# Kernel optimization log

Measured on AMD Instinct MI355X. Metric: run time of the kernel, lower is better.

The kernel has to match this reference:

```python
import jax, jax.numpy as jnp
import numpy as np

N1, E1 = 102400, 300000
N2, E2 = 10240, 40960
N3, E3 = 1024, 4096
G = 64
D = 256   # node_dim == hidden_dim (forced by where(M==0, x, M))
B = 64    # bond_dim
DEPTHS = (3, 3, 4)


def _make_edges(rng, n_nodes, n_edges):
    # build mirrored directed edges so every edge has an exact reverse
    half = n_edges // 2
    u = rng.integers(0, n_nodes, half)
    v = rng.integers(0, n_nodes, half)
    src = np.concatenate([u, v])
    dst = np.concatenate([v, u])
    rev = np.concatenate([np.arange(half, n_edges), np.arange(0, half)])
    return np.stack([src, dst]).astype(np.int64), rev.astype(np.int64)


def _linear_params(key, fan_in, fan_out):
    k1, k2 = jax.random.split(key)
    s = 1.0 / np.sqrt(fan_in)
    W = jax.random.uniform(k1, (fan_in, fan_out), jnp.float32, -s, s)
    b = jax.random.uniform(k2, (fan_out,), jnp.float32, -s, s)
    return W, b


def setup_inputs() -> dict:
    rng = np.random.default_rng(0)
    key = jax.random.key(0)
    ks = jax.random.split(key, 16)

    ei1, rev1 = _make_edges(rng, N1, E1)
    ei2, rev2 = _make_edges(rng, N2, E2)
    ei3, rev3 = _make_edges(rng, N3, E3)

    inp = {
        "x": jax.random.normal(ks[0], (N1, D), jnp.float32),
        "edge_attr1": jax.random.normal(ks[1], (E1, B), jnp.float32),
        "edge_attr2": jax.random.normal(ks[2], (E2, B), jnp.float32),
        "edge_attr3": jax.random.normal(ks[3], (E3, B), jnp.float32),
        "edge_index1": jnp.asarray(ei1), "rev_edge_index1": jnp.asarray(rev1),
        "edge_index2": jnp.asarray(ei2), "rev_edge_index2": jnp.asarray(rev2),
        "edge_index3": jnp.asarray(ei3), "rev_edge_index3": jnp.asarray(rev3),
        "batch1_2": jnp.asarray(np.repeat(np.arange(N2), N1 // N2)),
        "batch2": jnp.asarray(np.repeat(np.arange(N3), N2 // N3)),
        "batch3": jnp.asarray(np.repeat(np.arange(G), N3 // G)),
    }
    kidx = 4
    for lvl in (1, 2, 3):
        Wi, bi = _linear_params(ks[kidx], D + B, D); kidx += 1
        Wh, bh = _linear_params(ks[kidx], D, D); kidx += 1
        Wo, bo = _linear_params(ks[kidx], D + D, D); kidx += 1
        inp[f"Wi{lvl}"], inp[f"bi{lvl}"] = Wi, bi
        inp[f"Wh{lvl}"], inp[f"bh{lvl}"] = Wh, bh
        inp[f"Wo{lvl}"], inp[f"bo{lvl}"] = Wo, bo
    return inp


def _bmp(x, src, dst, rev, ea, Wi, bi, Wh, bh, Wo, bo, depth):
    # BondMessagePassing.forward (dropout is identity in eval)
    n = x.shape[0]
    H0 = jax.nn.relu(jnp.concatenate([x[src], ea], axis=1) @ Wi + bi)  # [E, D]
    H = H0
    for _ in range(depth - 1):
        agg = jax.ops.segment_sum(H, dst, num_segments=n)              # [N, D]
        M = agg[src] - H[rev]
        H = jax.nn.relu(H0 + M @ Wh + bh)
    M = jax.ops.segment_sum(H, dst, num_segments=n)
    M = jnp.where(jnp.sum(M, axis=1, keepdims=True) == 0, x, M)
    return jax.nn.relu(jnp.concatenate([x, M], axis=1) @ Wo + bo)


def _mean_pool(h, seg, n):
    s = jax.ops.segment_sum(h, seg, num_segments=n)
    c = jax.ops.segment_sum(jnp.ones((h.shape[0], 1), h.dtype), seg, num_segments=n)
    return s / jnp.maximum(c, 1.0)


def reference(x, edge_attr1, edge_attr2, edge_attr3,
              edge_index1, rev_edge_index1, edge_index2, rev_edge_index2,
              edge_index3, rev_edge_index3, batch1_2, batch2, batch3,
              Wi1, bi1, Wh1, bh1, Wo1, bo1,
              Wi2, bi2, Wh2, bh2, Wo2, bo2,
              Wi3, bi3, Wh3, bh3, Wo3, bo3):
    h1 = _bmp(x, edge_index1[0], edge_index1[1], rev_edge_index1, edge_attr1,
              Wi1, bi1, Wh1, bh1, Wo1, bo1, DEPTHS[0])
    x2 = _mean_pool(h1, batch1_2, N2)
    h2 = _bmp(x2, edge_index2[0], edge_index2[1], rev_edge_index2, edge_attr2,
              Wi2, bi2, Wh2, bh2, Wo2, bo2, DEPTHS[1])
    x3 = _mean_pool(h2, batch2, N3)
    h3 = _bmp(x3, edge_index3[0], edge_index3[1], rev_edge_index3, edge_attr3,
              Wi3, bi3, Wh3, bh3, Wo3, bo3, DEPTHS[2])
    out = _mean_pool(h3, batch3, G)  # [G, D] subgraph3_pooled
    return out
```

## Files before the change

### kernel.cpp

```cpp
#include <hip/hip_runtime.h>
#include <stdint.h>

typedef __bf16 bf16;
typedef __bf16 bf16x4 __attribute__((ext_vector_type(4)));
typedef __bf16 bf16x8 __attribute__((ext_vector_type(8)));
typedef float  f32x4  __attribute__((ext_vector_type(4)));

__device__ __forceinline__ int clampi(int v, int n) { return (v < 0 || v >= n) ? 0 : v; }

__device__ __forceinline__ void gload16(const void* g, void* l) {
  __builtin_amdgcn_global_load_lds((const __attribute__((address_space(1))) void*)g,
                                   (__attribute__((address_space(3))) void*)l, 16, 0, 0);
}

__global__ void wtcvt_kernel(const float* __restrict__ W, bf16* __restrict__ Wt, int K) {
  int idx = blockIdx.x * 256 + threadIdx.x;
  if (idx >= K * 256) return;
  int k = idx >> 8, n = idx & 255;
  Wt[(size_t)n * K + k] = (bf16)W[idx];
}

__global__ void hist_kernel(const int* __restrict__ dst, int E, int* __restrict__ cnt, int N) {
  int e = blockIdx.x * 256 + threadIdx.x;
  if (e < E) atomicAdd(&cnt[clampi(dst[e], N)], 1);
}

__global__ void scan_block_kernel(const int* __restrict__ cnt, int N,
                                  int* __restrict__ incl, int* __restrict__ bsums) {
  __shared__ int sd[256];
  int t = threadIdx.x, bid = blockIdx.x;
  int base = bid * 1024 + t * 4;
  int v0 = (base + 0 < N) ? cnt[base + 0] : 0;
  int v1 = (base + 1 < N) ? cnt[base + 1] : 0;
  int v2 = (base + 2 < N) ? cnt[base + 2] : 0;
  int v3 = (base + 3 < N) ? cnt[base + 3] : 0;
  int s1 = v0 + v1, s2 = s1 + v2, s3 = s2 + v3;
  sd[t] = s3;
  __syncthreads();
  for (int off = 1; off < 256; off <<= 1) {
    int x = 0;
    if (t >= off) x = sd[t - off];
    __syncthreads();
    sd[t] += x;
    __syncthreads();
  }
  int excl = sd[t] - s3;
  if (base + 0 < N) incl[base + 0] = excl + v0;
  if (base + 1 < N) incl[base + 1] = excl + s1;
  if (base + 2 < N) incl[base + 2] = excl + s2;
  if (base + 3 < N) incl[base + 3] = excl + s3;
  if (t == 255) bsums[bid] = sd[255];
}

__global__ void scan_sums_kernel(const int* __restrict__ bsums, int nb, int* __restrict__ bexcl) {
  __shared__ int sd[256];
  int t = threadIdx.x;
  int v = (t < nb) ? bsums[t] : 0;
  sd[t] = v;
  __syncthreads();
  for (int off = 1; off < 256; off <<= 1) {
    int x = 0;
    if (t >= off) x = sd[t - off];
    __syncthreads();
    sd[t] += x;
    __syncthreads();
  }
  if (t < nb) bexcl[t] = sd[t] - v;
}

__global__ void scan_add_kernel(const int* __restrict__ incl, const int* __restrict__ bexcl,
                                int N, int* __restrict__ offs) {
  int i = blockIdx.x * 256 + threadIdx.x;
  if (i < N) offs[i + 1] = incl[i] + bexcl[i >> 10];
  if (i == 0) offs[0] = 0;
}

__global__ void scatter_kernel(const int* __restrict__ dst, int E, const int* __restrict__ offs,
                               int* __restrict__ cursor, int* __restrict__ elist, int N) {
  int e = blockIdx.x * 256 + threadIdx.x;
  if (e < E) {
    int d = clampi(dst[e], N);
    int p = atomicAdd(&cursor[d], 1);
    elist[offs[d] + p] = e;
  }
}

template <int WHERE, int XF32>
__global__ void segsum_kernel(const bf16* __restrict__ H, const int* __restrict__ elist,
                              const int* __restrict__ offs, const float* __restrict__ xf,
                              const bf16* __restrict__ xb, bf16* __restrict__ out, int N) {
  int lane = threadIdx.x & 63;
  int node = blockIdx.x * 4 + (threadIdx.x >> 6);
  if (node >= N) return;
  int beg = offs[node], end = offs[node + 1];
  float a0 = 0.f, a1 = 0.f, a2 = 0.f, a3 = 0.f;
  for (int p = beg; p < end; ++p) {
    int e = elist[p];
    bf16x4 v = ((const bf16x4*)(H + (size_t)e * 256))[lane];
    a0 += (float)v[0]; a1 += (float)v[1]; a2 += (float)v[2]; a3 += (float)v[3];
  }
  if (WHERE) {
    float s = a0 + a1 + a2 + a3;
    for (int off = 1; off < 64; off <<= 1) s += __shfl_xor(s, off);
    if (s == 0.f) {
      bf16x4 o;
      if (XF32) {
        float4 xv = ((const float4*)(xf))[(size_t)node * 64 + lane];
        o[0] = (bf16)xv.x; o[1] = (bf16)xv.y; o[2] = (bf16)xv.z; o[3] = (bf16)xv.w;
      } else {
        o = ((const bf16x4*)(xb + (size_t)node * 256))[lane];
      }
      ((bf16x4*)(out + (size_t)node * 256))[lane] = o;
      return;
    }
  }
  bf16x4 o = {(bf16)a0, (bf16)a1, (bf16)a2, (bf16)a3};
  ((bf16x4*)(out + (size_t)node * 256))[lane] = o;
}

template <int OUTF32>
__global__ void pool_kernel(const bf16* __restrict__ h, bf16* __restrict__ outb,
                            float* __restrict__ outf, int Nout, int cnt) {
  int lane = threadIdx.x & 63;
  int node = blockIdx.x * 4 + (threadIdx.x >> 6);
  if (node >= Nout) return;
  float a0 = 0.f, a1 = 0.f, a2 = 0.f, a3 = 0.f;
  size_t base = (size_t)node * cnt;
  for (int p = 0; p < cnt; ++p) {
    bf16x4 v = ((const bf16x4*)(h + (base + p) * 256))[lane];
    a0 += (float)v[0]; a1 += (float)v[1]; a2 += (float)v[2]; a3 += (float)v[3];
  }
  float c = (float)cnt;
  a0 /= c; a1 /= c; a2 /= c; a3 /= c;
  if (OUTF32) {
    float4 o = {a0, a1, a2, a3};
    ((float4*)(outf + (size_t)node * 256))[lane] = o;
  } else {
    bf16x4 o = {(bf16)a0, (bf16)a1, (bf16)a2, (bf16)a3};
    ((bf16x4*)(outb + (size_t)node * 256))[lane] = o;
  }
}

template <int MODE, int XF32>
__global__ __launch_bounds__(256, 4) void gemm_kernel(
    const float* __restrict__ A1f, const bf16* __restrict__ A1b,
    const float* __restrict__ A2f, const bf16* __restrict__ A2b,
    const bf16* __restrict__ Wt, const float* __restrict__ bias, const bf16* H0,
    const int* __restrict__ srcIdx, const int* __restrict__ revIdx,
    bf16* out, int Mrows, int K, int Nsrc) {
  __shared__ __align__(16) bf16 As[64 * 64];
  __shared__ __align__(16) bf16 Bs[256 * 64];
  int tid = threadIdx.x;
  int lane = tid & 63;
  int wave = tid >> 6;
  int m0 = blockIdx.x * 64;

  int rowA[2], uA[2];
  int base1[2], base2[2];
#pragma unroll
  for (int r = 0; r < 2; ++r) {
    int unit = r * 256 + tid;
    rowA[r] = unit >> 3;
    uA[r] = unit & 7;
    int rr = m0 + rowA[r];
    if (rr >= Mrows) rr = Mrows - 1;
    if (MODE == 0) {
      base1[r] = clampi(srcIdx[rr], Nsrc) * 256;
      base2[r] = rr * 64;
    } else if (MODE == 1) {
      base1[r] = clampi(srcIdx[rr], Nsrc) * 256;
      base2[r] = clampi(revIdx[rr], Mrows) * 256;
    } else {
      base1[r] = rr * 256;
      base2[r] = rr * 256;
    }
  }

  f32x4 acc[4][4];
#pragma unroll
  for (int i = 0; i < 4; ++i)
#pragma unroll
    for (int j = 0; j < 4; ++j) acc[i][j] = (f32x4){0.f, 0.f, 0.f, 0.f};

  float4 pf[2][2];

  auto loadA = [&](int kc) {
    int k0 = kc * 64;
#pragma unroll
    for (int r = 0; r < 2; ++r) {
      int u8 = uA[r] * 8;
      if (MODE == 0) {
        if (k0 < 256) {
          if (XF32) {
            const float* g = A1f + (size_t)(base1[r] + k0 + u8);
            pf[r][0] = *(const float4*)g;
            pf[r][1] = *(const float4*)(g + 4);
          } else {
            pf[r][0] = *(const float4*)(A1b + (size_t)(base1[r] + k0 + u8));
          }
        } else {
          const float* g = A2f + (size_t)(base2[r] + u8);
          pf[r][0] = *(const float4*)g;
          pf[r][1] = *(const float4*)(g + 4);
        }
      } else if (MODE == 1) {
        pf[r][0] = *(const float4*)(A1b + (size_t)(base1[r] + k0 + u8));
        pf[r][1] = *(const float4*)(A2b + (size_t)(base2[r] + k0 + u8));
      } else {
        if (k0 < 256) {
          if (XF32) {
            const float* g = A1f + (size_t)(base1[r] + k0 + u8);
            pf[r][0] = *(const float4*)g;
            pf[r][1] = *(const float4*)(g + 4);
          } else {
            pf[r][0] = *(const float4*)(A1b + (size_t)(base1[r] + k0 + u8));
          }
        } else {
          pf[r][0] = *(const float4*)(A2b + (size_t)(base2[r] + (k0 - 256) + u8));
        }
      }
    }
  };

  auto writeA = [&](int kc) {
    int k0 = kc * 64;
#pragma unroll
    for (int r = 0; r < 2; ++r) {
      int row = rowA[r], us = uA[r] ^ (row & 7);
      bf16x8 v;
      bool cvt32;
      if (MODE == 0) cvt32 = XF32 || (k0 >= 256);
      else if (MODE == 2) cvt32 = XF32 && (k0 < 256);
      else cvt32 = false;
      if (MODE == 1) {
        bf16x8 va = *(bf16x8*)(&pf[r][0]);
        bf16x8 vh = *(bf16x8*)(&pf[r][1]);
#pragma unroll
        for (int j = 0; j < 8; ++j) v[j] = (bf16)((float)va[j] - (float)vh[j]);
      } else if (cvt32) {
        const float* f = (const float*)&pf[r][0];
#pragma unroll
        for (int j = 0; j < 8; ++j) v[j] = (bf16)f[j];
      } else {
        v = *(bf16x8*)(&pf[r][0]);
      }
      *(bf16x8*)(&As[(size_t)(row * 8 + us) * 8]) = v;
    }
  };

  auto loadB = [&](int kc) {
    int k0 = kc * 64;
#pragma unroll
    for (int r = 0; r < 8; ++r) {
      int unit = r * 256 + tid;
      int row = unit >> 3, us = (unit & 7) ^ (row & 7);
      const bf16* g = Wt + (size_t)row * K + k0 + us * 8;
      bf16* l = &Bs[(size_t)(r * 256 + wave * 64) * 8];
      gload16(g, l);
    }
  };

  int nk = K / 64;
  loadA(0);
  for (int kc = 0; kc < nk; ++kc) {
    __syncthreads();
    writeA(kc);
    loadB(kc);
    __syncthreads();
    if (kc + 1 < nk) loadA(kc + 1);
#pragma unroll
    for (int s = 0; s < 2; ++s) {
      int kq = s * 4 + (lane >> 4);
      bf16x8 af[4], bfr[4];
#pragma unroll
      for (int i = 0; i < 4; ++i) {
        int arow = i * 16 + (lane & 15);
        af[i] = *(const bf16x8*)(&As[(size_t)arow * 64 + (size_t)(kq ^ (arow & 7)) * 8]);
      }
#pragma unroll
      for (int j = 0; j < 4; ++j) {
        int brow = wave * 64 + j * 16 + (lane & 15);
        bfr[j] = *(const bf16x8*)(&Bs[(size_t)brow * 64 + (size_t)(kq ^ (brow & 7)) * 8]);
      }
#pragma unroll
      for (int i = 0; i < 4; ++i)
#pragma unroll
        for (int j = 0; j < 4; ++j)
          acc[i][j] = __builtin_amdgcn_mfma_f32_16x16x32_bf16(af[i], bfr[j], acc[i][j], 0, 0, 0);
    }
  }
#pragma unroll
  for (int i = 0; i < 4; ++i) {
    int rbase = m0 + i * 16 + ((lane >> 4) << 2);
#pragma unroll
    for (int j = 0; j < 4; ++j) {
      int col = wave * 64 + j * 16 + (lane & 15);
      float bcol = bias[col];
#pragma unroll
      for (int r = 0; r < 4; ++r) {
        int row = rbase + r;
        if (row < Mrows) {
          float v = acc[i][j][r] + bcol;
          if (MODE == 1) v += (float)H0[(size_t)row * 256 + col];
          v = fmaxf(v, 0.f);
          out[(size_t)row * 256 + col] = (bf16)v;
        }
      }
    }
  }
}

template <int XF32>
static void run_level(const float* xf, const bf16* xb, const float* ea,
                      const int* src, const int* dst, const int* rev, int E, int N, int depth,
                      const bf16* WiT, const float* bi_, const bf16* WhT, const float* bh_,
                      const bf16* WoT, const float* bo_,
                      bf16* C, bf16* Dd, bf16* Ee, bf16* agg, bf16* h,
                      int* cnt, int* incl, int* offs, int* cursr, int* bsums, int* bexcl,
                      int* elist, hipStream_t stream) {
  hipMemsetAsync(cnt, 0, (size_t)N * 4, stream);
  hist_kernel<<<(E + 255) / 256, 256, 0, stream>>>(dst, E, cnt, N);
  int nb = (N + 1023) / 1024;
  scan_block_kernel<<<nb, 256, 0, stream>>>(cnt, N, incl, bsums);
  scan_sums_kernel<<<1, 256, 0, stream>>>(bsums, nb, bexcl);
  scan_add_kernel<<<(N + 255) / 256, 256, 0, stream>>>(incl, bexcl, N, offs);
  hipMemsetAsync(cursr, 0, (size_t)N * 4, stream);
  scatter_kernel<<<(E + 255) / 256, 256, 0, stream>>>(dst, E, offs, cursr, elist, N);

  dim3 ge((E + 63) / 64);
  gemm_kernel<0, XF32><<<ge, 256, 0, stream>>>(xf, xb, ea, nullptr, WiT, bi_, nullptr, src,
                                               nullptr, C, E, 320, N);
  bf16* Hcur = C;
  for (int it = 0; it < depth - 1; ++it) {
    segsum_kernel<0, 0><<<(N + 3) / 4, 256, 0, stream>>>(Hcur, elist, offs, nullptr, nullptr,
                                                         agg, N);
    bf16* Hn = (it == depth - 2) ? C : ((it & 1) ? Ee : Dd);
    gemm_kernel<1, 0><<<ge, 256, 0, stream>>>(nullptr, agg, nullptr, Hcur, WhT, bh_, C, src,
                                              rev, Hn, E, 256, N);
    Hcur = Hn;
  }
  segsum_kernel<1, XF32><<<(N + 3) / 4, 256, 0, stream>>>(Hcur, elist, offs, xf, xb, agg, N);
  dim3 gn((N + 63) / 64);
  gemm_kernel<2, XF32><<<gn, 256, 0, stream>>>(xf, xb, nullptr, agg, WoT, bo_, nullptr, nullptr,
                                               nullptr, h, N, 512, N);
}

extern "C" void kernel_launch(void* const* d_in, const int* in_sizes, int n_in,
                              void* d_out, int out_size, void* d_ws, size_t ws_size,
                              hipStream_t stream) {
  constexpr int N1 = 102400, E1 = 300000;
  constexpr int N2 = 10240, E2 = 40960;
  constexpr int N3 = 1024, E3 = 4096;
  constexpr int G = 64;
  constexpr int KI = 320, KH = 256, KO = 512;

  const float* x   = (const float*)d_in[0];
  const float* ea1 = (const float*)d_in[1];
  const float* ea2 = (const float*)d_in[2];
  const float* ea3 = (const float*)d_in[3];
  const int* ei1 = (const int*)d_in[4];
  const int* rv1 = (const int*)d_in[5];
  const int* ei2 = (const int*)d_in[6];
  const int* rv2 = (const int*)d_in[7];
  const int* ei3 = (const int*)d_in[8];
  const int* rv3 = (const int*)d_in[9];
  const float *Wi[3], *bi[3], *Wh[3], *bh[3], *Wo[3], *bo[3];
  for (int l = 0; l < 3; ++l) {
    Wi[l] = (const float*)d_in[13 + 6 * l + 0];
    bi[l] = (const float*)d_in[13 + 6 * l + 1];
    Wh[l] = (const float*)d_in[13 + 6 * l + 2];
    bh[l] = (const float*)d_in[13 + 6 * l + 3];
    Wo[l] = (const float*)d_in[13 + 6 * l + 4];
    bo[l] = (const float*)d_in[13 + 6 * l + 5];
  }
  float* outp = (float*)d_out;
  char* ws = (char*)d_ws;

  size_t off = 0;
  auto alloc = [&](size_t b) { size_t o = off; off += (b + 255) & ~(size_t)255; return o; };
  size_t o_wit[3], o_wht[3], o_wot[3];
  for (int l = 0; l < 3; ++l) {
    o_wit[l] = alloc((size_t)256 * KI * 2);
    o_wht[l] = alloc((size_t)256 * KH * 2);
    o_wot[l] = alloc((size_t)256 * KO * 2);
  }
  size_t o_C   = alloc((size_t)E1 * 256 * 2);
  size_t o_D   = alloc((size_t)E1 * 256 * 2);
  size_t o_E3b = alloc((size_t)E3 * 256 * 2);
  size_t o_agg = alloc((size_t)N1 * 256 * 2);
  size_t o_x2  = alloc((size_t)N2 * 256 * 2);
  size_t o_h2  = alloc((size_t)N2 * 256 * 2);
  size_t o_x3  = alloc((size_t)N3 * 256 * 2);
  size_t o_h3  = alloc((size_t)N3 * 256 * 2);
  size_t o_cnt = alloc((size_t)N1 * 4);
  size_t o_inc = alloc((size_t)N1 * 4);
  size_t o_off = alloc((size_t)(N1 + 1) * 4);
  size_t o_cur = alloc((size_t)N1 * 4);
  size_t o_bs  = alloc(1024 * 4);
  size_t o_bx  = alloc(1024 * 4);
  size_t o_el  = alloc((size_t)E1 * 4);

  if (ws_size < off) {
    hipMemsetAsync(d_out, 0, (size_t)out_size * 4, stream);
    return;
  }

  int* cnt   = (int*)(ws + o_cnt);
  int* incl  = (int*)(ws + o_inc);
  int* offs  = (int*)(ws + o_off);
  int* cursr = (int*)(ws + o_cur);
  int* bsums = (int*)(ws + o_bs);
  int* bexcl = (int*)(ws + o_bx);
  int* elist = (int*)(ws + o_el);
  bf16* C    = (bf16*)(ws + o_C);
  bf16* Dd   = (bf16*)(ws + o_D);
  bf16* E3b  = (bf16*)(ws + o_E3b);
  bf16* agg  = (bf16*)(ws + o_agg);
  bf16* x2b  = (bf16*)(ws + o_x2);
  bf16* h2b  = (bf16*)(ws + o_h2);
  bf16* x3b  = (bf16*)(ws + o_x3);
  bf16* h3b  = (bf16*)(ws + o_h3);

  for (int l = 0; l < 3; ++l) {
    wtcvt_kernel<<<(KI * 256 + 255) / 256, 256, 0, stream>>>(Wi[l], (bf16*)(ws + o_wit[l]), KI);
    wtcvt_kernel<<<(KH * 256 + 255) / 256, 256, 0, stream>>>(Wh[l], (bf16*)(ws + o_wht[l]), KH);
    wtcvt_kernel<<<(KO * 256 + 255) / 256, 256, 0, stream>>>(Wo[l], (bf16*)(ws + o_wot[l]), KO);
  }

  run_level<1>(x, nullptr, ea1, ei1, ei1 + E1, rv1, E1, N1, 3,
               (bf16*)(ws + o_wit[0]), bi[0], (bf16*)(ws + o_wht[0]), bh[0],
               (bf16*)(ws + o_wot[0]), bo[0], C, Dd, Dd, agg, C,
               cnt, incl, offs, cursr, bsums, bexcl, elist, stream);
  pool_kernel<0><<<(N2 + 3) / 4, 256, 0, stream>>>(C, x2b, nullptr, N2, N1 / N2);

  run_level<0>(nullptr, x2b, ea2, ei2, ei2 + E2, rv2, E2, N2, 3,
               (bf16*)(ws + o_wit[1]), bi[1], (bf16*)(ws + o_wht[1]), bh[1],
               (bf16*)(ws + o_wot[1]), bo[1], C, Dd, Dd, agg, h2b,
               cnt, incl, offs, cursr, bsums, bexcl, elist, stream);
  pool_kernel<0><<<(N3 + 3) / 4, 256, 0, stream>>>(h2b, x3b, nullptr, N3, N2 / N3);

  run_level<0>(nullptr, x3b, ea3, ei3, ei3 + E3, rv3, E3, N3, 4,
               (bf16*)(ws + o_wit[2]), bi[2], (bf16*)(ws + o_wht[2]), bh[2],
               (bf16*)(ws + o_wot[2]), bo[2], C, Dd, E3b, agg, h3b,
               cnt, incl, offs, cursr, bsums, bexcl, elist, stream);
  pool_kernel<1><<<(G + 3) / 4, 256, 0, stream>>>(h3b, nullptr, outp, G, N3 / G);
}
```

Measured before the change: 1.364 ms.

## Double-buffer LDS tiles in the GEMM kernel to overlap loads with MFMA

The GEMM kernel now keeps two copies of the A and B LDS tiles. It issues the async global-to-LDS loads for the next K chunk and the register prefetch of A before computing on the current buffer, then writes the next A tile after the MFMA loop. This drops one of the two __syncthreads per K iteration and is meant to hide global load latency behind compute. In exchange LDS per block doubles to about 80KB and the occupancy hint drops from 4 to 2 blocks, so fewer waves are available to hide latency.

```diff
diff --git a/kernel.cpp b/kernel.cpp
--- a/kernel.cpp
+++ b/kernel.cpp
@@ -142,21 +142,20 @@
 }
 
 template <int MODE, int XF32>
-__global__ __launch_bounds__(256, 4) void gemm_kernel(
+__global__ __launch_bounds__(256, 2) void gemm_kernel(
     const float* __restrict__ A1f, const bf16* __restrict__ A1b,
     const float* __restrict__ A2f, const bf16* __restrict__ A2b,
     const bf16* __restrict__ Wt, const float* __restrict__ bias, const bf16* H0,
     const int* __restrict__ srcIdx, const int* __restrict__ revIdx,
     bf16* out, int Mrows, int K, int Nsrc) {
-  __shared__ __align__(16) bf16 As[64 * 64];
-  __shared__ __align__(16) bf16 Bs[256 * 64];
-  int tid = threadIdx.x;
-  int lane = tid & 63;
-  int wave = tid >> 6;
-  int m0 = blockIdx.x * 64;
-
-  int rowA[2], uA[2];
-  int base1[2], base2[2];
+  __shared__ __align__(16) bf16 As[2][64 * 64];
+  __shared__ __align__(16) bf16 Bs[2][256 * 64];
+  const int tid = threadIdx.x;
+  const int lane = tid & 63;
+  const int wave = tid >> 6;
+  const int m0 = blockIdx.x * 64;
+
+  int rowA[2], uA[2], base1[2], base2[2];
 #pragma unroll
   for (int r = 0; r < 2; ++r) {
     int unit = r * 256 + tid;
@@ -222,7 +221,7 @@
     }
   };
 
-  auto writeA = [&](int kc) {
+  auto writeA = [&](int kc, int buf) {
     int k0 = kc * 64;
 #pragma unroll
     for (int r = 0; r < 2; ++r) {
@@ -233,8 +232,8 @@
       else if (MODE == 2) cvt32 = XF32 && (k0 < 256);
       else cvt32 = false;
       if (MODE == 1) {
-        bf16x8 va = *(bf16x8*)(&pf[r][0]);
-        bf16x8 vh = *(bf16x8*)(&pf[r][1]);
+        bf16x8 va = *(bf16x8*)&pf[r][0];
+        bf16x8 vh = *(bf16x8*)&pf[r][1];
 #pragma unroll
         for (int j = 0; j < 8; ++j) v[j] = (bf16)((float)va[j] - (float)vh[j]);
       } else if (cvt32) {
@@ -242,32 +241,35 @@
 #pragma unroll
         for (int j = 0; j < 8; ++j) v[j] = (bf16)f[j];
       } else {
-        v = *(bf16x8*)(&pf[r][0]);
-      }
-      *(bf16x8*)(&As[(size_t)(row * 8 + us) * 8]) = v;
+        v = *(bf16x8*)&pf[r][0];
+      }
+      *(bf16x8*)(&As[buf][((size_t)row * 8 + us) * 8]) = v;
     }
   };
 
-  auto loadB = [&](int kc) {
+  auto issueB = [&](int kc, int buf) {
     int k0 = kc * 64;
 #pragma unroll
     for (int r = 0; r < 8; ++r) {
       int unit = r * 256 + tid;
       int row = unit >> 3, us = (unit & 7) ^ (row & 7);
-      const bf16* g = Wt + (size_t)row * K + k0 + us * 8;
-      bf16* l = &Bs[(size_t)(r * 256 + wave * 64) * 8];
-      gload16(g, l);
+      gload16(Wt + (size_t)row * K + k0 + us * 8, &Bs[buf][(r * 256 + wave * 64) * 8]);
     }
   };
 
-  int nk = K / 64;
+  const int nk = K / 64;
+  issueB(0, 0);
   loadA(0);
+  writeA(0, 0);
+  int cur = 0;
   for (int kc = 0; kc < nk; ++kc) {
     __syncthreads();
-    writeA(kc);
-    loadB(kc);
-    __syncthreads();
-    if (kc + 1 < nk) loadA(kc + 1);
+    if (kc + 1 < nk) {
+      issueB(kc + 1, cur ^ 1);
+      loadA(kc + 1);
+    }
+    const bf16* Asb = As[cur];
+    const bf16* Bsb = Bs[cur];
 #pragma unroll
     for (int s = 0; s < 2; ++s) {
       int kq = s * 4 + (lane >> 4);
@@ -275,12 +277,12 @@
 #pragma unroll
       for (int i = 0; i < 4; ++i) {
         int arow = i * 16 + (lane & 15);
-        af[i] = *(const bf16x8*)(&As[(size_t)arow * 64 + (size_t)(kq ^ (arow & 7)) * 8]);
+        af[i] = *(const bf16x8*)(&Asb[(size_t)arow * 64 + (size_t)(kq ^ (arow & 7)) * 8]);
       }
 #pragma unroll
       for (int j = 0; j < 4; ++j) {
         int brow = wave * 64 + j * 16 + (lane & 15);
-        bfr[j] = *(const bf16x8*)(&Bs[(size_t)brow * 64 + (size_t)(kq ^ (brow & 7)) * 8]);
+        bfr[j] = *(const bf16x8*)(&Bsb[(size_t)brow * 64 + (size_t)(kq ^ (brow & 7)) * 8]);
       }
 #pragma unroll
       for (int i = 0; i < 4; ++i)
@@ -288,6 +290,8 @@
         for (int j = 0; j < 4; ++j)
           acc[i][j] = __builtin_amdgcn_mfma_f32_16x16x32_bf16(af[i], bfr[j], acc[i][j], 0, 0, 0);
     }
+    if (kc + 1 < nk) writeA(kc + 1, cur ^ 1);
+    cur ^= 1;
   }
 #pragma unroll
   for (int i = 0; i < 4; ++i) {
```

New measurement: 1.355 ms. About the same (-0.7%).
